# Kernel optimization log

Measured on AMD Instinct MI355X. Metric: run time of the kernel, lower is better.

## Reference

```python
import jax, jax.numpy as jnp
import numpy as np

HEADS = 12
HEAD_SIZE = 64
NEG = 1e12


def _rope_tables(seq_len, head_size, dtype=jnp.float32):
    pos = jnp.arange(seq_len, dtype=dtype)[:, None]                      # [s,1]
    idx = jnp.arange(0, head_size, 2, dtype=dtype)                       # [hs/2]
    ang = pos / (10000.0 ** (idx / head_size))                           # [s,hs/2]
    sin = jnp.repeat(jnp.sin(ang), 2, axis=-1)                           # [s,hs]
    cos = jnp.repeat(jnp.cos(ang), 2, axis=-1)                           # [s,hs]
    return sin[None, :, None, :], cos[None, :, None, :]                  # [1,s,1,hs]


def _rotate_half_interleaved(x):
    # pairs (x0,x1) -> (-x1, x0), interleaved layout
    x2 = jnp.stack([-x[..., 1::2], x[..., ::2]], axis=-1)
    return x2.reshape(x.shape)


def setup_inputs() -> dict:
    key = jax.random.key(0)
    k1, k2, k3 = jax.random.split(key, 3)
    b, s, d = 8, 1024, 1024
    inputs = jax.random.normal(k1, (b, s, d), dtype=jnp.float32)
    W = jax.random.normal(k2, (d, HEADS * HEAD_SIZE * 2), dtype=jnp.float32) * 0.02
    bias = jnp.zeros((HEADS * HEAD_SIZE * 2,), dtype=jnp.float32)
    lengths = jax.random.randint(k3, (b,), s // 2, s + 1)
    mask = (jnp.arange(s)[None, :] < lengths[:, None]).astype(jnp.int32)  # [b,s]
    return {"inputs": inputs, "W": W, "bias": bias, "mask": mask}


def reference(inputs, W, bias, mask):
    b, s, _ = inputs.shape
    proj = inputs @ W + bias                                             # [b,s,2*h*hs]
    proj = proj.reshape(b, s, HEADS, 2 * HEAD_SIZE)
    qw, kw = proj[..., :HEAD_SIZE], proj[..., HEAD_SIZE:]
    sin, cos = _rope_tables(s, HEAD_SIZE, dtype=qw.dtype)
    qw = qw * cos + _rotate_half_interleaved(qw) * sin
    kw = kw * cos + _rotate_half_interleaved(kw) * sin
    logits = jnp.einsum('bmhd,bnhd->bhmn', qw, kw)                       # [b,h,m,n]
    m = mask.astype(logits.dtype)
    logits = logits - (1.0 - m)[:, None, None, :] * NEG                  # key padding
    logits = logits - (1.0 - m)[:, None, :, None] * NEG                  # query padding
    tri = (jnp.arange(s)[:, None] > jnp.arange(s)[None, :]).astype(logits.dtype)
    logits = logits - tri * NEG                                          # lower-tri (diag=-1)
    return logits / (HEAD_SIZE ** 0.5)
```

## Files before the change

kernel.cpp:

```cpp
#include <hip/hip_runtime.h>
#include <hip/hip_bf16.h>
#include <stdint.h>

#define NHEADS 12
#define HSZ 64
#define BATCH 8
#define SEQ 1024
#define DIN 1024
#define NPROJ 1536
#define MTOK 8192
#define NEGV 1e12f

typedef float  f32x4  __attribute__((ext_vector_type(4)));
typedef __bf16 bf16x8 __attribute__((ext_vector_type(8)));

__device__ __forceinline__ ushort f2bf(float x) {
  union { float f; uint32_t u; } v; v.f = x;
  uint32_t r = v.u + 0x7FFFu + ((v.u >> 16) & 1u);
  return (ushort)(r >> 16);
}

__device__ __forceinline__ void async16(const void* g, void* l) {
  __builtin_amdgcn_global_load_lds(
      (const __attribute__((address_space(1))) uint32_t*)g,
      (__attribute__((address_space(3))) uint32_t*)l,
      16, 0, 0);
}

__global__ __launch_bounds__(256) void k_prep(
    const float* __restrict__ inp, const float* __restrict__ W,
    ushort* __restrict__ A16, ushort* __restrict__ Wt, float* __restrict__ tab) {
  const int blk = blockIdx.x;
  const int tid = threadIdx.x;
  if (blk < 2048) {
    const float4* in4 = (const float4*)inp;
    ushort4* out4 = (ushort4*)A16;
    const int n4 = MTOK * DIN / 4;
    int i = blk * 256 + tid;
    for (; i < n4; i += 2048 * 256) {
      float4 v = in4[i];
      ushort4 o;
      o.x = f2bf(v.x); o.y = f2bf(v.y); o.z = f2bf(v.z); o.w = f2bf(v.w);
      out4[i] = o;
    }
  } else if (blk < 2432) {
    __shared__ float tile[64][65];
    const int bb = blk - 2048;
    const int n0 = (bb % 24) * 64;
    const int k0 = (bb / 24) * 64;
    const int c  = tid & 63;
    const int r0 = (tid >> 6) * 16;
    #pragma unroll
    for (int rr = 0; rr < 16; ++rr)
      tile[r0 + rr][c] = W[(size_t)(k0 + r0 + rr) * NPROJ + n0 + c];
    __syncthreads();
    #pragma unroll
    for (int rr = 0; rr < 16; ++rr)
      Wt[(size_t)(n0 + r0 + rr) * DIN + k0 + c] = f2bf(tile[c][r0 + rr]);
  } else {
    const int t = (blk - 2432) * 256 + tid;
    const int s = t >> 5, i = t & 31;
    const float p   = powf(10000.0f, (float)i / 32.0f);
    const float ang = (float)s / p;
    tab[2 * t]     = sinf(ang);
    tab[2 * t + 1] = cosf(ang);
  }
}

__global__ __launch_bounds__(256, 3) void k_gemm_proj(
    const ushort* __restrict__ A, const ushort* __restrict__ Bt,
    const float* __restrict__ bias, const float* __restrict__ tab,
    ushort* __restrict__ Qb, ushort* __restrict__ Kb) {
  __shared__ __align__(16) ushort As[2][128 * 32];
  __shared__ __align__(16) ushort Bs[2][128 * 32];
  const int tid  = threadIdx.x;
  const int lane = tid & 63;
  const int wid  = tid >> 6;
  const int wm = wid >> 1, wn = wid & 1;
  const int orig = blockIdx.x;
  const int wgid = (orig & 7) * 96 + (orig >> 3);
  const int m0 = (wgid / 12) * 128;
  const int n0 = (wgid % 12) * 128;

  const int off0 = tid * 16;
  const int off1 = 4096 + tid * 16;
  const int r0 = off0 >> 6, s0 = (off0 >> 4) & 3;
  const int r1 = off1 >> 6, s1 = (off1 >> 4) & 3;
  const int g0 = (s0 ^ ((r0 >> 1) & 3)) * 8;
  const int g1 = (s1 ^ ((r1 >> 1) & 3)) * 8;
  const ushort* gA0 = A  + (size_t)(m0 + r0) * DIN + g0;
  const ushort* gA1 = A  + (size_t)(m0 + r1) * DIN + g1;
  const ushort* gB0 = Bt + (size_t)(n0 + r0) * DIN + g0;
  const ushort* gB1 = Bt + (size_t)(n0 + r1) * DIN + g1;

  const int kb = lane >> 4;
  int aoff[4], boff[4];
  #pragma unroll
  for (int i = 0; i < 4; ++i) {
    const int ra = wm * 64 + i * 16 + (lane & 15);
    aoff[i] = ra * 32 + (kb ^ ((ra >> 1) & 3)) * 8;
    const int rb = wn * 64 + i * 16 + (lane & 15);
    boff[i] = rb * 32 + (kb ^ ((rb >> 1) & 3)) * 8;
  }

  f32x4 acc[4][4] = {};
  async16(gA0, As[0] + wid * 512);
  async16(gA1, As[0] + 2048 + wid * 512);
  async16(gB0, Bs[0] + wid * 512);
  async16(gB1, Bs[0] + 2048 + wid * 512);
  __syncthreads();

  int cur = 0;
  #pragma unroll 2
  for (int kt = 0; kt < DIN / 32; ++kt) {
    if (kt + 1 < DIN / 32) {
      const int ko = (kt + 1) * 32;
      ushort* ad = As[cur ^ 1];
      ushort* bd = Bs[cur ^ 1];
      async16(gA0 + ko, ad + wid * 512);
      async16(gA1 + ko, ad + 2048 + wid * 512);
      async16(gB0 + ko, bd + wid * 512);
      async16(gB1 + ko, bd + 2048 + wid * 512);
    }
    const ushort* ab = As[cur];
    const ushort* bb = Bs[cur];
    bf16x8 af[4], bfr[4];
    #pragma unroll
    for (int i = 0; i < 4; ++i) {
      af[i]  = *(const bf16x8*)(ab + aoff[i]);
      bfr[i] = *(const bf16x8*)(bb + boff[i]);
    }
    #pragma unroll
    for (int mi = 0; mi < 4; ++mi)
      #pragma unroll
      for (int ni = 0; ni < 4; ++ni)
        acc[mi][ni] = __builtin_amdgcn_mfma_f32_16x16x32_bf16(af[mi], bfr[ni], acc[mi][ni], 0, 0, 0);
    __syncthreads();
    cur ^= 1;
  }

  const int b = m0 >> 10;
  const int baserow = m0 + wm * 64 + ((lane >> 4) << 2);
  #pragma unroll
  for (int ni = 0; ni < 4; ++ni) {
    const int n = n0 + wn * 64 + ni * 16 + (lane & 15);
    const float bv = bias[n];
    const int h  = n >> 7;
    const int c  = n & 127;
    const int d  = c & 63;
    const int pi = d >> 1;
    ushort* dst = ((c < 64) ? Qb : Kb) + (size_t)(b * NHEADS + h) * SEQ * 64 + d;
    #pragma unroll
    for (int mi = 0; mi < 4; ++mi) {
      #pragma unroll
      for (int j = 0; j < 4; ++j) {
        const int gm = baserow + mi * 16 + j;
        const int s  = gm & (SEQ - 1);
        float v = acc[mi][ni][j] + bv;
        float p = __shfl_xor(v, 1);
        float2 sc = ((const float2*)tab)[s * 32 + pi];
        float o = (d & 1) ? fmaf(v, sc.y, p * sc.x) : fmaf(v, sc.y, -p * sc.x);
        dst[(size_t)s * 64] = f2bf(o);
      }
    }
  }
}

__global__ __launch_bounds__(256) void k_out(
    const ushort* __restrict__ Qb, const ushort* __restrict__ Kb,
    const int* __restrict__ mask, float* __restrict__ out) {
  __shared__ __align__(16) ushort Qs[128 * 64];
  __shared__ __align__(16) ushort Ks[128 * 64];
  const int tid  = threadIdx.x;
  const int orig = blockIdx.x;
  const int wgid = (orig & 7) * 768 + (orig >> 3);
  const int bh = wgid >> 6;
  const int b  = bh / NHEADS;
  const int mi_ = (wgid >> 3) & 7;
  const int ni_ = wgid & 7;
  const int m0 = mi_ * 128;
  const int n0 = ni_ * 128;
  const int* mb = mask + b * SEQ;
  float* ob = out + (size_t)bh * SEQ * SEQ;

  if (mi_ > ni_) {
    const int c0 = (tid & 31) * 4;
    const int r0 = tid >> 5;
    f32x4 np4;
    #pragma unroll
    for (int j = 0; j < 4; ++j) np4[j] = mb[n0 + c0 + j] ? 0.0f : NEGV;
    for (int r = r0; r < 128; r += 8) {
      const int gm = m0 + r;
      const float mp = (mb[gm] ? 0.0f : NEGV) + NEGV;
      f32x4 v;
      #pragma unroll
      for (int j = 0; j < 4; ++j) v[j] = -(np4[j] + mp) * 0.125f;
      __builtin_nontemporal_store(v, (f32x4*)(ob + (size_t)gm * SEQ + n0 + c0));
    }
    return;
  }

  const int lane = tid & 63;
  const int wid  = tid >> 6;
  const int wm = wid >> 1, wn = wid & 1;
  const ushort* Qt = Qb + (size_t)bh * SEQ * 64;
  const ushort* Kt = Kb + (size_t)bh * SEQ * 64;

  #pragma unroll
  for (int is = 0; is < 4; ++is) {
    const int off = is * 4096 + tid * 16;
    const int row = off >> 7;
    const int g8  = ((((off >> 4) & 7) ^ (row & 7))) * 8;
    async16(Qt + (size_t)(m0 + row) * 64 + g8, Qs + is * 2048 + wid * 512);
    async16(Kt + (size_t)(n0 + row) * 64 + g8, Ks + is * 2048 + wid * 512);
  }
  __syncthreads();

  f32x4 acc[4][4] = {};
  const int kb = lane >> 4;
  #pragma unroll
  for (int ks = 0; ks < 2; ++ks) {
    bf16x8 qf[4], kf[4];
    #pragma unroll
    for (int i = 0; i < 4; ++i) {
      const int rq = wm * 64 + i * 16 + (lane & 15);
      qf[i] = *(const bf16x8*)(Qs + rq * 64 + ((ks * 4 + kb) ^ (rq & 7)) * 8);
      const int rk = wn * 64 + i * 16 + (lane & 15);
      kf[i] = *(const bf16x8*)(Ks + rk * 64 + ((ks * 4 + kb) ^ (rk & 7)) * 8);
    }
    #pragma unroll
    for (int mi = 0; mi < 4; ++mi)
      #pragma unroll
      for (int ni = 0; ni < 4; ++ni)
        acc[mi][ni] = __builtin_amdgcn_mfma_f32_16x16x32_bf16(qf[mi], kf[ni], acc[mi][ni], 0, 0, 0);
  }

  const int mrow0 = m0 + wm * 64 + ((lane >> 4) << 2);
  const int ncol0 = n0 + wn * 64 + (lane & 15);
  float npen[4];
  int gn_[4];
  #pragma unroll
  for (int ni = 0; ni < 4; ++ni) {
    gn_[ni]  = ncol0 + ni * 16;
    npen[ni] = mb[gn_[ni]] ? 0.0f : NEGV;
  }
  #pragma unroll
  for (int mi = 0; mi < 4; ++mi) {
    #pragma unroll
    for (int j = 0; j < 4; ++j) {
      const int gm = mrow0 + mi * 16 + j;
      const float mpen = mb[gm] ? 0.0f : NEGV;
      float* orow = ob + (size_t)gm * SEQ;
      #pragma unroll
      for (int ni = 0; ni < 4; ++ni) {
        const int gn = gn_[ni];
        const float tpen = (gm > gn) ? NEGV : 0.0f;
        orow[gn] = (acc[mi][ni][j] - (mpen + npen[ni] + tpen)) * 0.125f;
      }
    }
  }
}

extern "C" void kernel_launch(void* const* d_in, const int* in_sizes, int n_in,
                              void* d_out, int out_size, void* d_ws, size_t ws_size,
                              hipStream_t stream) {
  const float* inp  = (const float*)d_in[0];
  const float* W    = (const float*)d_in[1];
  const float* bias = (const float*)d_in[2];
  const int*   mask = (const int*)d_in[3];
  float* out = (float*)d_out;

  char* ws = (char*)d_ws;
  ushort* A16  = (ushort*)ws;
  ushort* WT16 = (ushort*)(ws + 16777216);
  float*  tab  = (float*)(ws + 19922944);
  ushort* Qb   = (ushort*)(ws + 20185088);
  ushort* Kb   = (ushort*)(ws + 32768000);

  k_prep<<<2560, 256, 0, stream>>>(inp, W, A16, WT16, tab);
  k_gemm_proj<<<768, 256, 0, stream>>>(A16, WT16, bias, tab, Qb, Kb);
  k_out<<<6144, 256, 0, stream>>>(Qb, Kb, mask, out);
}
```

Measured before the change: 119.2 us.

## Triple-buffer projection GEMM LDS with one barrier per k-step

Moves the projection GEMM from double-buffered to triple-buffered LDS staging. Loads are issued two k-steps ahead, and a partial vmcnt wait plus a single barrier replaces the trailing __syncthreads. The aim is to hide global-load latency and remove one block-wide barrier per iteration. It raises LDS use from 32KB to 48KB per block, which may cut occupancy below the 3 blocks per CU set in launch_bounds. Correctness depends on the hand-written waitcnt counts.

```diff
diff --git a/kernel.cpp b/kernel.cpp
--- a/kernel.cpp
+++ b/kernel.cpp
@@ -71,8 +71,8 @@
     const ushort* __restrict__ A, const ushort* __restrict__ Bt,
     const float* __restrict__ bias, const float* __restrict__ tab,
     ushort* __restrict__ Qb, ushort* __restrict__ Kb) {
-  __shared__ __align__(16) ushort As[2][128 * 32];
-  __shared__ __align__(16) ushort Bs[2][128 * 32];
+  __shared__ __align__(16) ushort As[3][128 * 32];
+  __shared__ __align__(16) ushort Bs[3][128 * 32];
   const int tid  = threadIdx.x;
   const int lane = tid & 63;
   const int wid  = tid >> 6;
@@ -103,40 +103,54 @@
     boff[i] = rb * 32 + (kb ^ ((rb >> 1) & 3)) * 8;
   }
 
+  const int lA = wid * 512;
+  const int lB = 2048 + wid * 512;
+
+  ushort *a0 = As[0], *a1 = As[1], *a2 = As[2];
+  ushort *b0 = Bs[0], *b1 = Bs[1], *b2 = Bs[2];
+
   f32x4 acc[4][4] = {};
-  async16(gA0, As[0] + wid * 512);
-  async16(gA1, As[0] + 2048 + wid * 512);
-  async16(gB0, Bs[0] + wid * 512);
-  async16(gB1, Bs[0] + 2048 + wid * 512);
-  __syncthreads();
-
-  int cur = 0;
-  #pragma unroll 2
-  for (int kt = 0; kt < DIN / 32; ++kt) {
-    if (kt + 1 < DIN / 32) {
-      const int ko = (kt + 1) * 32;
-      ushort* ad = As[cur ^ 1];
-      ushort* bd = Bs[cur ^ 1];
-      async16(gA0 + ko, ad + wid * 512);
-      async16(gA1 + ko, ad + 2048 + wid * 512);
-      async16(gB0 + ko, bd + wid * 512);
-      async16(gB1 + ko, bd + 2048 + wid * 512);
-    }
-    const ushort* ab = As[cur];
-    const ushort* bb = Bs[cur];
+  async16(gA0,      a0 + lA); async16(gA1,      a0 + lB);
+  async16(gB0,      b0 + lA); async16(gB1,      b0 + lB);
+  async16(gA0 + 32, a1 + lA); async16(gA1 + 32, a1 + lB);
+  async16(gB0 + 32, b1 + lA); async16(gB1 + 32, b1 + lB);
+
+  for (int kt = 0; kt < 31; ++kt) {
+    asm volatile("s_waitcnt vmcnt(4)" ::: "memory");
+    __builtin_amdgcn_s_barrier();
+    if (kt < 30) {
+      const int ko = (kt + 2) * 32;
+      async16(gA0 + ko, a2 + lA); async16(gA1 + ko, a2 + lB);
+      async16(gB0 + ko, b2 + lA); async16(gB1 + ko, b2 + lB);
+    }
     bf16x8 af[4], bfr[4];
     #pragma unroll
     for (int i = 0; i < 4; ++i) {
-      af[i]  = *(const bf16x8*)(ab + aoff[i]);
-      bfr[i] = *(const bf16x8*)(bb + boff[i]);
+      af[i]  = *(const bf16x8*)(a0 + aoff[i]);
+      bfr[i] = *(const bf16x8*)(b0 + boff[i]);
     }
     #pragma unroll
     for (int mi = 0; mi < 4; ++mi)
       #pragma unroll
       for (int ni = 0; ni < 4; ++ni)
         acc[mi][ni] = __builtin_amdgcn_mfma_f32_16x16x32_bf16(af[mi], bfr[ni], acc[mi][ni], 0, 0, 0);
-    __syncthreads();
-    cur ^= 1;
+    ushort* ta = a0; a0 = a1; a1 = a2; a2 = ta;
+    ushort* tb = b0; b0 = b1; b1 = b2; b2 = tb;
+  }
+  asm volatile("s_waitcnt vmcnt(0)" ::: "memory");
+  __builtin_amdgcn_s_barrier();
+  {
+    bf16x8 af[4], bfr[4];
+    #pragma unroll
+    for (int i = 0; i < 4; ++i) {
+      af[i]  = *(const bf16x8*)(a0 + aoff[i]);
+      bfr[i] = *(const bf16x8*)(b0 + boff[i]);
+    }
+    #pragma unroll
+    for (int mi = 0; mi < 4; ++mi)
+      #pragma unroll
+      for (int ni = 0; ni < 4; ++ni)
+        acc[mi][ni] = __builtin_amdgcn_mfma_f32_16x16x32_bf16(af[mi], bfr[ni], acc[mi][ni], 0, 0, 0);
   }
 
   const int b = m0 >> 10;
```

Measured after the change: 118.2 us. Within noise of the previous version (-0.8%).
